# Performance work log

Hardware: AMD Instinct MI355X
Metric: run time of the kernel (lower is better)

Reference implementation:

```python
import jax, jax.numpy as jnp
import numpy as np
from jax import lax

# Module config (matches init_kwargs)
C_IN, C_OUT, D_STATE = 512, 256, 16
D_INNER = 2 * C_OUT          # canonical Mamba expand=2
DT_RANK = C_OUT // 16        # ceil(256/16) = 16
D_CONV = 4
BN_EPS = 1e-5


def setup_inputs() -> dict:
    key = jax.random.key(0)
    ks = jax.random.split(key, 16)
    s = 0.02
    B, H, W = 8, 64, 64
    inp = {
        "x": jax.random.normal(ks[0], (B, C_IN, H, W), jnp.float32),
        # lateral 1x1 conv
        "lateral_w": jax.random.normal(ks[1], (C_OUT, C_IN), jnp.float32) * s,
        "lateral_b": jnp.zeros((C_OUT,), jnp.float32),
        # mamba block params
        "in_proj_w": jax.random.normal(ks[2], (2 * D_INNER, C_OUT), jnp.float32) * s,
        "conv1d_w": jax.random.normal(ks[3], (D_INNER, D_CONV), jnp.float32) * s,
        "conv1d_b": jnp.zeros((D_INNER,), jnp.float32),
        "x_proj_w": jax.random.normal(ks[4], (DT_RANK + 2 * D_STATE, D_INNER), jnp.float32) * s,
        "dt_proj_w": jax.random.normal(ks[5], (D_INNER, DT_RANK), jnp.float32) * s,
        "dt_proj_b": jnp.full((D_INNER,), -4.0, jnp.float32),  # softplus -> small dt
        "A_log": jnp.log(jnp.broadcast_to(jnp.arange(1, D_STATE + 1, dtype=jnp.float32), (D_INNER, D_STATE))),  # S4D-real init
        "D_param": jnp.ones((D_INNER,), jnp.float32),
        "out_proj_w": jax.random.normal(ks[6], (C_OUT, D_INNER), jnp.float32) * s,
        # refine: 3x3 conv + BN (eval) + ReLU
        "refine_w": jax.random.normal(ks[7], (C_OUT, C_OUT, 3, 3), jnp.float32) * s,
        "refine_b": jnp.zeros((C_OUT,), jnp.float32),
        "bn_gamma": jnp.ones((C_OUT,), jnp.float32),
        "bn_beta": jnp.zeros((C_OUT,), jnp.float32),
        "bn_mean": jnp.zeros((C_OUT,), jnp.float32),
        "bn_var": jnp.ones((C_OUT,), jnp.float32),
    }
    return inp


def _silu(v):
    return v * jax.nn.sigmoid(v)


def _mamba(u, in_proj_w, conv1d_w, conv1d_b, x_proj_w, dt_proj_w, dt_proj_b,
           A_log, D_param, out_proj_w):
    """Canonical Mamba block on u: (B, L, D) -> (B, L, D)."""
    B, L, D = u.shape
    xz = jnp.einsum('bld,ed->ble', u, in_proj_w)            # (B,L,2*d_inner)
    xm, z = jnp.split(xz, 2, axis=-1)
    # causal depthwise conv1d over L
    xc = xm.transpose(0, 2, 1)                               # (B,d_inner,L)
    xc = lax.conv_general_dilated(xc, conv1d_w[:, None, :], (1,),
                                  [(D_CONV - 1, 0)],
                                  feature_group_count=D_INNER)
    xc = _silu(xc + conv1d_b[None, :, None]).transpose(0, 2, 1)  # (B,L,d_inner)
    proj = jnp.einsum('bld,ed->ble', xc, x_proj_w)           # (B,L,dt_rank+2*N)
    dt_r = proj[..., :DT_RANK]
    B_ssm = proj[..., DT_RANK:DT_RANK + D_STATE]             # (B,L,N)
    C_ssm = proj[..., DT_RANK + D_STATE:]                    # (B,L,N)
    dt = jax.nn.softplus(jnp.einsum('blr,dr->bld', dt_r, dt_proj_w) + dt_proj_b)
    A = -jnp.exp(A_log)                                      # (d_inner,N)

    def step(h, inputs):
        dt_t, B_t, C_t, x_t = inputs                         # (B,d), (B,N), (B,N), (B,d)
        dA = jnp.exp(dt_t[..., None] * A)                    # (B,d,N)
        h = dA * h + dt_t[..., None] * B_t[:, None, :] * x_t[..., None]
        y = jnp.einsum('bdn,bn->bd', h, C_t)
        return h, y

    xs = (dt.transpose(1, 0, 2), B_ssm.transpose(1, 0, 2),
          C_ssm.transpose(1, 0, 2), xc.transpose(1, 0, 2))
    h0 = jnp.zeros((B, D_INNER, D_STATE), u.dtype)
    _, ys = lax.scan(step, h0, xs)                           # (L,B,d_inner)
    y = ys.transpose(1, 0, 2) + xc * D_param
    y = y * _silu(z)
    return jnp.einsum('ble,de->bld', y, out_proj_w)          # (B,L,D)


def reference(x, lateral_w, lateral_b, in_proj_w, conv1d_w, conv1d_b, x_proj_w,
              dt_proj_w, dt_proj_b, A_log, D_param, out_proj_w, refine_w,
              refine_b, bn_gamma, bn_beta, bn_mean, bn_var):
    B, _, H, W = x.shape
    # lateral 1x1 conv
    xl = jnp.einsum('oi,bihw->bohw', lateral_w, x) + lateral_b[None, :, None, None]
    # mamba on flattened spatial sequence, residual add
    u = xl.reshape(B, C_OUT, H * W).transpose(0, 2, 1)        # (B,L,C)
    m = _mamba(u, in_proj_w, conv1d_w, conv1d_b, x_proj_w, dt_proj_w,
               dt_proj_b, A_log, D_param, out_proj_w)
    xr = xl + m.transpose(0, 2, 1).reshape(B, C_OUT, H, W)
    # refine: 3x3 conv + BN(eval) + ReLU
    r = lax.conv_general_dilated(xr, refine_w, (1, 1), [(1, 1), (1, 1)])
    r = r + refine_b[None, :, None, None]
    inv = bn_gamma / jnp.sqrt(bn_var + BN_EPS)
    r = (r - bn_mean[None, :, None, None]) * inv[None, :, None, None] + bn_beta[None, :, None, None]
    return jax.nn.relu(r)
```

## Files before the change

### kernel.cpp

```cpp
#include <hip/hip_runtime.h>
#include <math.h>

#define NB   8
#define CIN  512
#define COUT 256
#define DIN  512
#define LHW  4096
#define NCHK 64
#define CHL  64
#define PW   66
#define PPOS (PW*PW)

typedef __attribute__((ext_vector_type(8))) short bf16x8;
typedef __attribute__((ext_vector_type(4))) float f32x4;

__device__ __forceinline__ float siluf(float v)  { return v / (1.f + __expf(-v)); }
__device__ __forceinline__ float splusf(float v) { return v > 20.f ? v : log1pf(__expf(v)); }

__device__ __forceinline__ unsigned short f2b(float f) {
  union { float f; unsigned u; } v; v.f = f;
  unsigned r = v.u + 0x7fff + ((v.u >> 16) & 1);
  return (unsigned short)(r >> 16);
}
__device__ __forceinline__ float b2f(unsigned int u) {
  union { unsigned u; float f; } v; v.u = (u & 0xffffu) << 16; return v.f;
}

__device__ __forceinline__ void gload16(const unsigned short* g, unsigned short* l) {
  __builtin_amdgcn_global_load_lds(
      (const __attribute__((address_space(1))) unsigned int*)g,
      (__attribute__((address_space(3))) unsigned int*)l, 16, 0, 0);
}

#define WO1 131072
#define WO2 393216
#define WO3 425984
#define WO4 557056
__global__ __launch_bounds__(256)
void k_wprep(const float* __restrict__ lw, const float* __restrict__ ipw,
             const float* __restrict__ xpw, const float* __restrict__ opw,
             const float* __restrict__ rw, unsigned short* __restrict__ wb) {
  const int i = blockIdx.x * 256 + threadIdx.x;
  if (i < WO1)      wb[i] = f2b(lw[i]);
  else if (i < WO2) wb[i] = f2b(ipw[i - WO1]);
  else if (i < WO3) {
    const int j = i - WO2, row = j >> 9, col = j & 511;
    wb[i] = (row < 48) ? f2b(xpw[row * 512 + col]) : (unsigned short)0;
  }
  else if (i < WO4) wb[i] = f2b(opw[i - WO3]);
  else {
    const int j = i - WO4, o = j / 2304, kk = j % 2304;
    const int tap = kk >> 8, ch = kk & 255;
    wb[i] = f2b(rw[(o * 256 + ch) * 9 + tap]);
  }
}

__global__ __launch_bounds__(256)
void k_xpose(const float* __restrict__ x, unsigned short* __restrict__ xt) {
  __shared__ unsigned short Ts[64][80];
  const int b  = blockIdx.z;
  const int k0 = blockIdx.y * 64;
  const int l0 = blockIdx.x * 64;
  const int t  = threadIdx.x;
  const int tx = t & 15, ty = t >> 4;
#pragma unroll
  for (int r = 0; r < 4; ++r) {
    const int k = ty + r * 16;
    float4 v = *(const float4*)(x + ((size_t)b * CIN + k0 + k) * LHW + l0 + tx * 4);
    Ts[tx*4+0][k] = f2b(v.x);
    Ts[tx*4+1][k] = f2b(v.y);
    Ts[tx*4+2][k] = f2b(v.z);
    Ts[tx*4+3][k] = f2b(v.w);
  }
  __syncthreads();
  const int lr = t >> 2, kc = (t & 3) * 16;
  unsigned short* dst = xt + ((size_t)b * LHW + l0 + lr) * CIN + k0 + kc;
  *(uint4*)dst       = *(const uint4*)&Ts[lr][kc];
  *(uint4*)(dst + 8) = *(const uint4*)&Ts[lr][kc + 8];
}

template<int RSA, int RSB, int KTOT>
__device__ __forceinline__ void gemm_loop_128(
    const unsigned short* __restrict__ Ab, const unsigned short* __restrict__ Bb,
    unsigned short* As, unsigned short* Bs, int t, f32x4 acc[4][4]) {
  const int w = t >> 6, lane = t & 63;
  const int wm = w >> 1, wn = w & 1;
  const int arow = t >> 2, acol = (t & 3) * 8;
  const int fr = lane & 15, g8 = (lane >> 4) * 8;
  for (int k0 = 0; k0 < KTOT; k0 += 32) {
    __syncthreads();
    gload16(Ab + (size_t)arow * RSA + k0 + acol,        &As[w * 512]);
    gload16(Ab + (size_t)(64 + arow) * RSA + k0 + acol, &As[2048 + w * 512]);
    gload16(Bb + (size_t)arow * RSB + k0 + acol,        &Bs[w * 512]);
    gload16(Bb + (size_t)(64 + arow) * RSB + k0 + acol, &Bs[2048 + w * 512]);
    __syncthreads();
    bf16x8 af[4], bf[4];
#pragma unroll
    for (int f = 0; f < 4; ++f) {
      af[f] = *(const bf16x8*)&As[(wm*64 + f*16 + fr) * 32 + g8];
      bf[f] = *(const bf16x8*)&Bs[(wn*64 + f*16 + fr) * 32 + g8];
    }
#pragma unroll
    for (int i = 0; i < 4; ++i)
#pragma unroll
      for (int j = 0; j < 4; ++j)
        acc[i][j] = __builtin_amdgcn_mfma_f32_16x16x32_bf16(af[i], bf[j], acc[i][j], 0, 0, 0);
  }
}

__global__ __launch_bounds__(256)
void k_lat_mfma(const unsigned short* __restrict__ xt, const unsigned short* __restrict__ lwb,
                const float* __restrict__ lb, unsigned short* __restrict__ ub) {
  __shared__ __align__(16) unsigned short As[4096], Bs[4096];
  const int t = threadIdx.x, lane = t & 63, w = t >> 6;
  const int wm = w >> 1, wn = w & 1;
  const int b = blockIdx.z, m0 = blockIdx.y * 128, n0 = blockIdx.x * 128;
  f32x4 acc[4][4] = {};
  gemm_loop_128<512, 512, 512>(xt + ((size_t)b * LHW + m0) * 512,
                               lwb + (size_t)n0 * 512, As, Bs, t, acc);
  const int fr = lane & 15, q4 = (lane >> 4) * 4;
#pragma unroll
  for (int i = 0; i < 4; ++i) {
    const int l = m0 + wm*64 + i*16 + q4;
#pragma unroll
    for (int j = 0; j < 4; ++j) {
      const int o = n0 + wn*64 + j*16 + fr;
      const float bias = lb[o];
      unsigned short* dst = ub + ((size_t)b * LHW + l) * COUT + o;
#pragma unroll
      for (int q = 0; q < 4; ++q)
        dst[(size_t)q * COUT] = f2b(acc[i][j][q] + bias);
    }
  }
}

__global__ __launch_bounds__(256)
void k_inproj_mfma(const unsigned short* __restrict__ ub, const unsigned short* __restrict__ ipwb,
                   unsigned short* __restrict__ xm_b, unsigned short* __restrict__ zsb) {
  __shared__ __align__(16) unsigned short As[4096], Bs[4096];
  const int t = threadIdx.x, lane = t & 63, w = t >> 6;
  const int wm = w >> 1, wn = w & 1;
  const int b = blockIdx.z, m0 = blockIdx.y * 128, n0 = blockIdx.x * 128;
  f32x4 acc[4][4] = {};
  gemm_loop_128<256, 256, 256>(ub + ((size_t)b * LHW + m0) * 256,
                               ipwb + (size_t)n0 * 256, As, Bs, t, acc);
  const int fr = lane & 15, q4 = (lane >> 4) * 4;
  const bool isz = (n0 >= 512);
#pragma unroll
  for (int i = 0; i < 4; ++i) {
    const int l = m0 + wm*64 + i*16 + q4;
#pragma unroll
    for (int j = 0; j < 4; ++j) {
      const int e = n0 + wn*64 + j*16 + fr;
      if (isz) {
        unsigned short* dst = zsb + ((size_t)b * LHW + l) * DIN + (e - 512);
#pragma unroll
        for (int q = 0; q < 4; ++q)
          dst[(size_t)q * DIN] = f2b(siluf(acc[i][j][q]));
      } else {
        unsigned short* dst = xm_b + ((size_t)b * LHW + l) * DIN + e;
#pragma unroll
        for (int q = 0; q < 4; ++q)
          dst[(size_t)q * DIN] = f2b(acc[i][j][q]);
      }
    }
  }
}

__global__ __launch_bounds__(256)
void k_conv1d(const unsigned short* __restrict__ xm_b, const float* __restrict__ cw,
              const float* __restrict__ cb, unsigned short* __restrict__ xc_b) {
  const int tid = blockIdx.x * 256 + threadIdx.x;
  const int e8 = tid & 63;
  const int l  = (tid >> 6) & 4095;
  const int b  = tid >> 18;
  const int e0 = e8 * 8;
  float acc[8];
  *(float4*)&acc[0] = *(const float4*)(cb + e0);
  *(float4*)&acc[4] = *(const float4*)(cb + e0 + 4);
  float wv[8][4];
#pragma unroll
  for (int q = 0; q < 8; ++q) {
    float4 w4 = *(const float4*)(cw + (e0 + q) * 4);
    wv[q][0] = w4.x; wv[q][1] = w4.y; wv[q][2] = w4.z; wv[q][3] = w4.w;
  }
  const unsigned short* base = xm_b + (size_t)b * LHW * DIN + e0;
#pragma unroll
  for (int k = 0; k < 4; ++k) {
    const int ll = l - 3 + k;
    if (ll >= 0) {
      uint4 raw = *(const uint4*)(base + (size_t)ll * DIN);
      acc[0] = fmaf(b2f(raw.x),       wv[0][k], acc[0]);
      acc[1] = fmaf(b2f(raw.x >> 16), wv[1][k], acc[1]);
      acc[2] = fmaf(b2f(raw.y),       wv[2][k], acc[2]);
      acc[3] = fmaf(b2f(raw.y >> 16), wv[3][k], acc[3]);
      acc[4] = fmaf(b2f(raw.z),       wv[4][k], acc[4]);
      acc[5] = fmaf(b2f(raw.z >> 16), wv[5][k], acc[5]);
      acc[6] = fmaf(b2f(raw.w),       wv[6][k], acc[6]);
      acc[7] = fmaf(b2f(raw.w >> 16), wv[7][k], acc[7]);
    }
  }
  uint4 o;
  o.x = (unsigned)f2b(siluf(acc[0])) | ((unsigned)f2b(siluf(acc[1])) << 16);
  o.y = (unsigned)f2b(siluf(acc[2])) | ((unsigned)f2b(siluf(acc[3])) << 16);
  o.z = (unsigned)f2b(siluf(acc[4])) | ((unsigned)f2b(siluf(acc[5])) << 16);
  o.w = (unsigned)f2b(siluf(acc[6])) | ((unsigned)f2b(siluf(acc[7])) << 16);
  *(uint4*)(xc_b + ((size_t)b * LHW + l) * DIN + e0) = o;
}

__global__ __launch_bounds__(256)
void k_xproj_mfma(const unsigned short* __restrict__ xc_b, const unsigned short* __restrict__ xpwb,
                  float* __restrict__ proj) {
  __shared__ __align__(16) unsigned short As[4096], Bs[2048];
  const int t = threadIdx.x, lane = t & 63, w = t >> 6;
  const int wm = w >> 1, wn = w & 1;
  const int b = blockIdx.y, m0 = blockIdx.x * 128;
  const int arow = t >> 2, acol = (t & 3) * 8;
  const int fr = lane & 15, g8 = (lane >> 4) * 8;
  const unsigned short* Ab = xc_b + ((size_t)b * LHW + m0) * 512;
  f32x4 acc[4][2] = {};
  for (int k0 = 0; k0 < 512; k0 += 32) {
    __syncthreads();
    gload16(Ab + (size_t)arow * 512 + k0 + acol,        &As[w * 512]);
    gload16(Ab + (size_t)(64 + arow) * 512 + k0 + acol, &As[2048 + w * 512]);
    gload16(xpwb + (size_t)arow * 512 + k0 + acol,      &Bs[w * 512]);
    __syncthreads();
    bf16x8 af[4], bf[2];
#pragma unroll
    for (int f = 0; f < 4; ++f)
      af[f] = *(const bf16x8*)&As[(wm*64 + f*16 + fr) * 32 + g8];
#pragma unroll
    for (int f = 0; f < 2; ++f)
      bf[f] = *(const bf16x8*)&Bs[(wn*32 + f*16 + fr) * 32 + g8];
#pragma unroll
    for (int i = 0; i < 4; ++i)
#pragma unroll
      for (int j = 0; j < 2; ++j)
        acc[i][j] = __builtin_amdgcn_mfma_f32_16x16x32_bf16(af[i], bf[j], acc[i][j], 0, 0, 0);
  }
  const int q4 = (lane >> 4) * 4;
#pragma unroll
  for (int i = 0; i < 4; ++i) {
    const int l = m0 + wm*64 + i*16 + q4;
#pragma unroll
    for (int j = 0; j < 2; ++j) {
      const int col = wn*32 + j*16 + fr;
      if (col < 48) {
        float* dst = proj + ((size_t)b * LHW + l) * 48 + col;
#pragma unroll
        for (int q = 0; q < 4; ++q)
          dst[(size_t)q * 48] = acc[i][j][q];
      }
    }
  }
}

__global__ __launch_bounds__(512)
void k_dt(const float* __restrict__ proj, const float* __restrict__ dtpw,
          const float* __restrict__ dtpb, unsigned short* __restrict__ dtb) {
  __shared__ float prs[32 * 16];
  const int d = threadIdx.x;
  const size_t l0 = (size_t)blockIdx.x * 32;
  for (int i = d; i < 32 * 4; i += 512) {
    const int row = i >> 2, c4 = i & 3;
    *(float4*)&prs[row * 16 + c4 * 4] = *(const float4*)(proj + (l0 + row) * 48 + c4 * 4);
  }
  float w[16];
#pragma unroll
  for (int q = 0; q < 4; ++q)
    *(float4*)(&w[q*4]) = *(const float4*)(dtpw + d * 16 + q * 4);
  const float bias = dtpb[d];
  __syncthreads();
#pragma unroll 4
  for (int i = 0; i < 32; ++i) {
    const float* pr = &prs[i * 16];
    float4 r0 = *(const float4*)pr;
    float4 r1 = *(const float4*)(pr + 4);
    float4 r2 = *(const float4*)(pr + 8);
    float4 r3 = *(const float4*)(pr + 12);
    float a0 = fmaf(w[0], r0.x, fmaf(w[1],  r0.y, fmaf(w[2],  r0.z, w[3]  * r0.w)));
    float a1 = fmaf(w[4], r1.x, fmaf(w[5],  r1.y, fmaf(w[6],  r1.z, w[7]  * r1.w)));
    float a2 = fmaf(w[8], r2.x, fmaf(w[9],  r2.y, fmaf(w[10], r2.z, w[11] * r2.w)));
    float a3 = fmaf(w[12],r3.x, fmaf(w[13], r3.y, fmaf(w[14], r3.z, w[15] * r3.w)));
    dtb[(l0 + i) * 512 + d] = f2b(splusf(bias + ((a0 + a1) + (a2 + a3))));
  }
}

__global__ __launch_bounds__(512, 4)
void k_scanA(const float* __restrict__ proj, const unsigned short* __restrict__ dtb,
             const unsigned short* __restrict__ xc_b,
             const float* __restrict__ A_log, float* __restrict__ PS) {
  __shared__ float prs[CHL * 16];
  const int bx = blockIdx.x;
  const int b = bx >> 6, c = bx & 63;
  const int d = threadIdx.x;
  const size_t rbase = (size_t)b * LHW + c * CHL;
  for (int i = d; i < CHL * 4; i += 512) {
    const int row = i >> 2, c4 = i & 3;
    *(float4*)&prs[row * 16 + c4 * 4] = *(const float4*)(proj + (rbase + row) * 48 + 16 + c4 * 4);
  }
  float An[16], h[16];
#pragma unroll
  for (int q = 0; q < 4; ++q) {
    float4 a4 = *(const float4*)(A_log + d*16 + q*4);
    An[q*4+0] = -__expf(a4.x); An[q*4+1] = -__expf(a4.y);
    An[q*4+2] = -__expf(a4.z); An[q*4+3] = -__expf(a4.w);
  }
#pragma unroll
  for (int n = 0; n < 16; ++n) h[n] = 0.f;
  const float An0 = An[0];
  bool lin = true;
#pragma unroll
  for (int n = 1; n < 16; ++n)
    lin = lin && (fabsf(An[n] - (n + 1) * An0) <= 1e-4f * fabsf(An[n]));
  float sdt = 0.f;
  const unsigned short* dt0 = dtb + rbase * 512 + d;
  const unsigned short* xc0 = xc_b + rbase * DIN + d;
  __syncthreads();
  for (int i = 0; i < CHL; ++i) {
    const float dt = b2f(dt0[(size_t)i * 512]);
    sdt += dt;
    const float dtx = dt * b2f(xc0[(size_t)i * DIN]);
    float dA[16];
    if (lin) {
      const float e1 = __expf(dt * An0);
      const float e2 = e1 * e1, e3 = e2 * e1, e4 = e2 * e2;
      dA[0] = e1; dA[1] = e2; dA[2] = e3; dA[3] = e4;
#pragma unroll
      for (int n = 4; n < 16; ++n) dA[n] = dA[n-4] * e4;
    } else {
#pragma unroll
      for (int n = 0; n < 16; ++n) dA[n] = __expf(dt * An[n]);
    }
    const float* pr = &prs[i * 16];
#pragma unroll
    for (int q = 0; q < 4; ++q) {
      float4 B4 = *(const float4*)(pr + q*4);
      h[q*4+0] = fmaf(dA[q*4+0], h[q*4+0], dtx * B4.x);
      h[q*4+1] = fmaf(dA[q*4+1], h[q*4+1], dtx * B4.y);
      h[q*4+2] = fmaf(dA[q*4+2], h[q*4+2], dtx * B4.z);
      h[q*4+3] = fmaf(dA[q*4+3], h[q*4+3], dtx * B4.w);
    }
  }
  float* o = PS + ((size_t)bx * 512 + d) * 32;
#pragma unroll
  for (int q = 0; q < 4; ++q)
    *(float4*)(o + q*4) = make_float4(__expf(sdt*An[q*4+0]), __expf(sdt*An[q*4+1]),
                                      __expf(sdt*An[q*4+2]), __expf(sdt*An[q*4+3]));
#pragma unroll
  for (int q = 0; q < 4; ++q)
    *(float4*)(o + 16 + q*4) = make_float4(h[q*4], h[q*4+1], h[q*4+2], h[q*4+3]);
}

__global__ __launch_bounds__(256)
void k_scanB(const float* __restrict__ PS, float* __restrict__ hst) {
  const int tid = blockIdx.x * 256 + threadIdx.x;
  const int n = tid & 15;
  const int d = (tid >> 4) & 511;
  const int b = tid >> 13;
  float h = 0.f;
  for (int c = 0; c < NCHK; ++c) {
    const size_t idx = (size_t)((b*NCHK + c)*512 + d);
    hst[idx*16 + n] = h;
    h = PS[idx*32 + n] * h + PS[idx*32 + 16 + n];
  }
}

__global__ __launch_bounds__(512, 4)
void k_scanC(const float* __restrict__ proj, const unsigned short* __restrict__ dtb,
             const unsigned short* __restrict__ xc_b,
             const unsigned short* __restrict__ zsb, const float* __restrict__ hst,
             const float* __restrict__ A_log, const float* __restrict__ Dpar,
             unsigned short* __restrict__ ydata) {
  __shared__ float prs[CHL * 32];
  const int bx = blockIdx.x;
  const int b = bx >> 6, c = bx & 63;
  const int d = threadIdx.x;
  const size_t rbase = (size_t)b * LHW + c * CHL;
  for (int i = d; i < CHL * 8; i += 512) {
    const int row = i >> 3, c4 = i & 7;
    *(float4*)&prs[row * 32 + c4 * 4] = *(const float4*)(proj + (rbase + row) * 48 + 16 + c4 * 4);
  }
  float An[16], h[16];
#pragma unroll
  for (int q = 0; q < 4; ++q) {
    float4 a4 = *(const float4*)(A_log + d*16 + q*4);
    An[q*4+0] = -__expf(a4.x); An[q*4+1] = -__expf(a4.y);
    An[q*4+2] = -__expf(a4.z); An[q*4+3] = -__expf(a4.w);
  }
#pragma unroll
  for (int q = 0; q < 4; ++q) {
    float4 h4 = *(const float4*)(hst + ((size_t)bx * 512 + d) * 16 + q*4);
    h[q*4+0] = h4.x; h[q*4+1] = h4.y; h[q*4+2] = h4.z; h[q*4+3] = h4.w;
  }
  const float An0 = An[0];
  bool lin = true;
#pragma unroll
  for (int n = 1; n < 16; ++n)
    lin = lin && (fabsf(An[n] - (n + 1) * An0) <= 1e-4f * fabsf(An[n]));
  const float dp = Dpar[d];
  const unsigned short* dt0 = dtb + rbase * 512 + d;
  const unsigned short* xc0 = xc_b + rbase * DIN + d;
  const unsigned short* zs0 = zsb + rbase * DIN + d;
  unsigned short* y0 = ydata + rbase * DIN + d;
  __syncthreads();
  for (int i = 0; i < CHL; ++i) {
    const float dt = b2f(dt0[(size_t)i * 512]);
    const float xt = b2f(xc0[(size_t)i * DIN]);
    const float zv = b2f(zs0[(size_t)i * DIN]);
    const float dtx = dt * xt;
    float dA[16];
    if (lin) {
      const float e1 = __expf(dt * An0);
      const float e2 = e1 * e1, e3 = e2 * e1, e4 = e2 * e2;
      dA[0] = e1; dA[1] = e2; dA[2] = e3; dA[3] = e4;
#pragma unroll
      for (int n = 4; n < 16; ++n) dA[n] = dA[n-4] * e4;
    } else {
#pragma unroll
      for (int n = 0; n < 16; ++n) dA[n] = __expf(dt * An[n]);
    }
    const float* pr = &prs[i * 32];
    float y0a = 0.f, y1a = 0.f, y2a = 0.f, y3a = 0.f;
#pragma unroll
    for (int q = 0; q < 4; ++q) {
      float4 B4 = *(const float4*)(pr + q*4);
      float4 C4 = *(const float4*)(pr + 16 + q*4);
      h[q*4+0] = fmaf(dA[q*4+0], h[q*4+0], dtx * B4.x);
      h[q*4+1] = fmaf(dA[q*4+1], h[q*4+1], dtx * B4.y);
      h[q*4+2] = fmaf(dA[q*4+2], h[q*4+2], dtx * B4.z);
      h[q*4+3] = fmaf(dA[q*4+3], h[q*4+3], dtx * B4.w);
      y0a = fmaf(h[q*4+0], C4.x, y0a);
      y1a = fmaf(h[q*4+1], C4.y, y1a);
      y2a = fmaf(h[q*4+2], C4.z, y2a);
      y3a = fmaf(h[q*4+3], C4.w, y3a);
    }
    const float y = (y0a + y1a) + (y2a + y3a);
    y0[(size_t)i * DIN] = f2b((y + xt * dp) * zv);
  }
}

__global__ __launch_bounds__(256)
void k_outproj_mfma(const unsigned short* __restrict__ ydata, const unsigned short* __restrict__ opwb,
                    const unsigned short* __restrict__ ub, unsigned short* __restrict__ xrp) {
  __shared__ __align__(16) unsigned short As[4096], Bs[4096];
  const int t = threadIdx.x, lane = t & 63, w = t >> 6;
  const int wm = w >> 1, wn = w & 1;
  const int b = blockIdx.z, m0 = blockIdx.y * 128, n0 = blockIdx.x * 128;
  f32x4 acc[4][4] = {};
  gemm_loop_128<512, 512, 512>(ydata + ((size_t)b * LHW + m0) * 512,
                               opwb + (size_t)n0 * 512, As, Bs, t, acc);
  const int fr = lane & 15, q4 = (lane >> 4) * 4;
#pragma unroll
  for (int i = 0; i < 4; ++i) {
    const int lbase = m0 + wm*64 + i*16 + q4;
#pragma unroll
    for (int q = 0; q < 4; ++q) {
      const int l = lbase + q;
      const int pos = ((l >> 6) + 1) * PW + (l & 63) + 1;
#pragma unroll
      for (int j = 0; j < 4; ++j) {
        const int o = n0 + wn*64 + j*16 + fr;
        const float r = b2f(ub[((size_t)b * LHW + l) * COUT + o]);
        xrp[((size_t)b * PPOS + pos) * COUT + o] = f2b(acc[i][j][q] + r);
      }
    }
  }
}

__global__ __launch_bounds__(256)
void k_refine_mfma(const unsigned short* __restrict__ Aw,
                   const unsigned short* __restrict__ xrp,
                   const float* __restrict__ rb, const float* __restrict__ bng,
                   const float* __restrict__ bnb, const float* __restrict__ bnm,
                   const float* __restrict__ bnv, float* __restrict__ out) {
  __shared__ __align__(16) unsigned short As[4096], Bs[4096];
  const int t = threadIdx.x;
  const int lane = t & 63;
  const int w = t >> 6;
  const int wm = w >> 1, wn = w & 1;
  const int b  = blockIdx.z;
  const int m0 = blockIdx.y * 128;
  const int n0 = blockIdx.x * 128;
  const int y0 = n0 >> 6;
  const unsigned short* xb = xrp + (size_t)b * PPOS * COUT;
  const int arow = t >> 2;
  const int acol = (t & 3) * 8;
  f32x4 acc[4][4] = {};
  for (int ks = 0; ks < 72; ++ks) {
    const int tap = ks >> 3;
    const int i0  = (ks & 7) * 32;
    const int ky  = tap / 3, kx = tap - ky * 3;
    const int k0  = tap * 256 + i0;
    const unsigned short* ga0 = Aw + (size_t)(m0 + arow) * 2304 + k0 + acol;
    const unsigned short* gb0 = xb + ((size_t)((y0 + ky) * PW + kx + arow)) * COUT + i0 + acol;
    __syncthreads();
    gload16(ga0,              &As[w * 512]);
    gload16(ga0 + 64 * 2304,  &As[2048 + w * 512]);
    gload16(gb0,              &Bs[w * 512]);
    gload16(gb0 + PW * COUT,  &Bs[2048 + w * 512]);
    __syncthreads();
    const int fr = lane & 15, g8 = (lane >> 4) * 8;
    bf16x8 af[4], bfr[4];
#pragma unroll
    for (int f = 0; f < 4; ++f) {
      af[f]  = *(const bf16x8*)&As[(wm*64 + f*16 + fr) * 32 + g8];
      bfr[f] = *(const bf16x8*)&Bs[(wn*64 + f*16 + fr) * 32 + g8];
    }
#pragma unroll
    for (int i = 0; i < 4; ++i)
#pragma unroll
      for (int j = 0; j < 4; ++j)
        acc[i][j] = __builtin_amdgcn_mfma_f32_16x16x32_bf16(af[i], bfr[j], acc[i][j], 0, 0, 0);
  }
  const int fr = lane & 15, q4 = (lane >> 4) * 4;
#pragma unroll
  for (int i = 0; i < 4; ++i) {
    const int obase = m0 + wm*64 + i*16 + q4;
#pragma unroll
    for (int q = 0; q < 4; ++q) {
      const int o = obase + q;
      const float inv = bng[o] * rsqrtf(bnv[o] + 1e-5f);
      const float sh  = (rb[o] - bnm[o]) * inv + bnb[o];
      float* orow = out + ((size_t)b * COUT + o) * LHW + n0 + wn*64 + fr;
#pragma unroll
      for (int j = 0; j < 4; ++j)
        orow[j*16] = fmaxf(fmaf(acc[i][j][q], inv, sh), 0.f);
    }
  }
}

extern "C" void kernel_launch(void* const* d_in, const int* in_sizes, int n_in,
                              void* d_out, int out_size, void* d_ws, size_t ws_size,
                              hipStream_t stream) {
  const float* x    = (const float*)d_in[0];
  const float* lw   = (const float*)d_in[1];
  const float* lb   = (const float*)d_in[2];
  const float* ipw  = (const float*)d_in[3];
  const float* cw   = (const float*)d_in[4];
  const float* cb   = (const float*)d_in[5];
  const float* xpw  = (const float*)d_in[6];
  const float* dtpw = (const float*)d_in[7];
  const float* dtpb = (const float*)d_in[8];
  const float* Alog = (const float*)d_in[9];
  const float* Dpar = (const float*)d_in[10];
  const float* opw  = (const float*)d_in[11];
  const float* rw   = (const float*)d_in[12];
  const float* rb   = (const float*)d_in[13];
  const float* bng  = (const float*)d_in[14];
  const float* bnb  = (const float*)d_in[15];
  const float* bnm  = (const float*)d_in[16];
  const float* bnv  = (const float*)d_in[17];
  float* out = (float*)d_out;

  float* ws = (float*)d_ws;
  unsigned short* ub   = (unsigned short*)ws;
  unsigned short* xt   = (unsigned short*)(ws + 4194304);
  unsigned short* xm_b = (unsigned short*)(ws + 12582912);
  unsigned short* xc_b = (unsigned short*)(ws + 20971520);
  unsigned short* zsb  = (unsigned short*)(ws + 29360128);
  float* proj = ws + 46137344;
  float* PS   = ws + 47710208;
  float* hst  = ws + 56098816;
  unsigned short* wb = (unsigned short*)(ws + 60293120);
  unsigned short* lwb  = wb;
  unsigned short* ipwb = wb + WO1;
  unsigned short* xpwb = wb + WO2;
  unsigned short* opwb = wb + WO3;
  unsigned short* Aw   = wb + WO4;
  unsigned short* ydata = xm_b;
  unsigned short* dtb   = xt;
  unsigned short* xrp   = xt;

  k_wprep<<<dim3(4480), 256, 0, stream>>>(lw, ipw, xpw, opw, rw, wb);
  k_xpose<<<dim3(64, 8, 8), 256, 0, stream>>>(x, xt);
  k_lat_mfma<<<dim3(2, 32, 8), 256, 0, stream>>>(xt, lwb, lb, ub);
  k_inproj_mfma<<<dim3(8, 32, 8), 256, 0, stream>>>(ub, ipwb, xm_b, zsb);
  k_conv1d<<<dim3(8192), 256, 0, stream>>>(xm_b, cw, cb, xc_b);
  k_xproj_mfma<<<dim3(32, 8), 256, 0, stream>>>(xc_b, xpwb, proj);
  k_dt<<<dim3(NB * LHW / 32), 512, 0, stream>>>(proj, dtpw, dtpb, dtb);
  k_scanA<<<dim3(NB * NCHK), 512, 0, stream>>>(proj, dtb, xc_b, Alog, PS);
  k_scanB<<<dim3(256), 256, 0, stream>>>(PS, hst);
  k_scanC<<<dim3(NB * NCHK), 512, 0, stream>>>(proj, dtb, xc_b, zsb, hst, Alog, Dpar, ydata);
  hipMemsetAsync(xrp, 0, (size_t)NB * PPOS * COUT * sizeof(unsigned short), stream);
  k_outproj_mfma<<<dim3(2, 32, 8), 256, 0, stream>>>(ydata, opwb, ub, xrp);
  k_refine_mfma<<<dim3(32, 2, 8), 256, 0, stream>>>(Aw, xrp, rb, bng, bnb, bnm, bnv, out);
}
```

Before: 411.8 us.

## Fold dt_proj into x_proj weights, fuse dt GEMM, halve scan chunk length

A new prep kernel precomputes dt_proj_w·x_proj_w[:16] as a fused 512x512 bf16 weight, stacked on the B/C rows of x_proj. One MFMA GEMM then produces both softplus(dt) in bf16 and the B/C projections, which removes the separate k_dt kernel and its reread of proj. The cost is a larger GEMM (N padded to 640 instead of 64), and rounding the fused weights to bf16 changes dt numerics. Softplus is also rewritten in a stable max+log(1+exp(-|v|)) form, and the scan now uses 128 chunks of 32 to give more parallel blocks at the price of a longer serial carry pass.

```diff
diff --git a/kernel.cpp b/kernel.cpp
--- a/kernel.cpp
+++ b/kernel.cpp
@@ -6,8 +6,8 @@
 #define COUT 256
 #define DIN  512
 #define LHW  4096
-#define NCHK 64
-#define CHL  64
+#define NCHK 128
+#define CHL  32
 #define PW   66
 #define PPOS (PW*PW)
 
@@ -15,7 +15,9 @@
 typedef __attribute__((ext_vector_type(4))) float f32x4;
 
 __device__ __forceinline__ float siluf(float v)  { return v / (1.f + __expf(-v)); }
-__device__ __forceinline__ float splusf(float v) { return v > 20.f ? v : log1pf(__expf(v)); }
+__device__ __forceinline__ float splusf(float v) {
+  return fmaxf(v, 0.f) + __logf(1.f + __expf(-fabsf(v)));
+}
 
 __device__ __forceinline__ unsigned short f2b(float f) {
   union { float f; unsigned u; } v; v.f = f;
@@ -53,6 +55,22 @@
     const int tap = kk >> 8, ch = kk & 255;
     wb[i] = f2b(rw[(o * 256 + ch) * 9 + tap]);
   }
+}
+
+__global__ __launch_bounds__(256)
+void k_wfuse(const float* __restrict__ dtpw, const float* __restrict__ xpw,
+             unsigned short* __restrict__ wfb) {
+  const int tid = blockIdx.x * 256 + threadIdx.x;
+  const int row = tid >> 9, e = tid & 511;
+  float v = 0.f;
+  if (row < 512) {
+#pragma unroll
+    for (int r = 0; r < 16; ++r)
+      v = fmaf(dtpw[row * 16 + r], xpw[r * 512 + e], v);
+  } else if (row < 560) {
+    v = xpw[(row - 512) * 512 + e];
+  }
+  wfb[tid] = f2b(v);
 }
 
 __global__ __launch_bounds__(256)
@@ -209,80 +227,36 @@
 }
 
 __global__ __launch_bounds__(256)
-void k_xproj_mfma(const unsigned short* __restrict__ xc_b, const unsigned short* __restrict__ xpwb,
-                  float* __restrict__ proj) {
-  __shared__ __align__(16) unsigned short As[4096], Bs[2048];
+void k_xdt_mfma(const unsigned short* __restrict__ xc_b, const unsigned short* __restrict__ wfb,
+                const float* __restrict__ dtpb,
+                unsigned short* __restrict__ dtb, float* __restrict__ proj) {
+  __shared__ __align__(16) unsigned short As[4096], Bs[4096];
   const int t = threadIdx.x, lane = t & 63, w = t >> 6;
   const int wm = w >> 1, wn = w & 1;
-  const int b = blockIdx.y, m0 = blockIdx.x * 128;
-  const int arow = t >> 2, acol = (t & 3) * 8;
-  const int fr = lane & 15, g8 = (lane >> 4) * 8;
-  const unsigned short* Ab = xc_b + ((size_t)b * LHW + m0) * 512;
-  f32x4 acc[4][2] = {};
-  for (int k0 = 0; k0 < 512; k0 += 32) {
-    __syncthreads();
-    gload16(Ab + (size_t)arow * 512 + k0 + acol,        &As[w * 512]);
-    gload16(Ab + (size_t)(64 + arow) * 512 + k0 + acol, &As[2048 + w * 512]);
-    gload16(xpwb + (size_t)arow * 512 + k0 + acol,      &Bs[w * 512]);
-    __syncthreads();
-    bf16x8 af[4], bf[2];
-#pragma unroll
-    for (int f = 0; f < 4; ++f)
-      af[f] = *(const bf16x8*)&As[(wm*64 + f*16 + fr) * 32 + g8];
-#pragma unroll
-    for (int f = 0; f < 2; ++f)
-      bf[f] = *(const bf16x8*)&Bs[(wn*32 + f*16 + fr) * 32 + g8];
-#pragma unroll
-    for (int i = 0; i < 4; ++i)
-#pragma unroll
-      for (int j = 0; j < 2; ++j)
-        acc[i][j] = __builtin_amdgcn_mfma_f32_16x16x32_bf16(af[i], bf[j], acc[i][j], 0, 0, 0);
-  }
-  const int q4 = (lane >> 4) * 4;
+  const int b = blockIdx.z, m0 = blockIdx.x * 128, n0 = blockIdx.y * 128;
+  f32x4 acc[4][4] = {};
+  gemm_loop_128<512, 512, 512>(xc_b + ((size_t)b * LHW + m0) * 512,
+                               wfb + (size_t)n0 * 512, As, Bs, t, acc);
+  const int fr = lane & 15, q4 = (lane >> 4) * 4;
 #pragma unroll
   for (int i = 0; i < 4; ++i) {
     const int l = m0 + wm*64 + i*16 + q4;
 #pragma unroll
-    for (int j = 0; j < 2; ++j) {
-      const int col = wn*32 + j*16 + fr;
-      if (col < 48) {
-        float* dst = proj + ((size_t)b * LHW + l) * 48 + col;
+    for (int j = 0; j < 4; ++j) {
+      const int c = n0 + wn*64 + j*16 + fr;
+      if (c < 512) {
+        const float bias = dtpb[c];
+        unsigned short* dst = dtb + ((size_t)b * LHW + l) * 512 + c;
+#pragma unroll
+        for (int q = 0; q < 4; ++q)
+          dst[(size_t)q * 512] = f2b(splusf(acc[i][j][q] + bias));
+      } else if (c < 560) {
+        float* dst = proj + ((size_t)b * LHW + l) * 48 + (c - 512);
 #pragma unroll
         for (int q = 0; q < 4; ++q)
           dst[(size_t)q * 48] = acc[i][j][q];
       }
     }
-  }
-}
-
-__global__ __launch_bounds__(512)
-void k_dt(const float* __restrict__ proj, const float* __restrict__ dtpw,
-          const float* __restrict__ dtpb, unsigned short* __restrict__ dtb) {
-  __shared__ float prs[32 * 16];
-  const int d = threadIdx.x;
-  const size_t l0 = (size_t)blockIdx.x * 32;
-  for (int i = d; i < 32 * 4; i += 512) {
-    const int row = i >> 2, c4 = i & 3;
-    *(float4*)&prs[row * 16 + c4 * 4] = *(const float4*)(proj + (l0 + row) * 48 + c4 * 4);
-  }
-  float w[16];
-#pragma unroll
-  for (int q = 0; q < 4; ++q)
-    *(float4*)(&w[q*4]) = *(const float4*)(dtpw + d * 16 + q * 4);
-  const float bias = dtpb[d];
-  __syncthreads();
-#pragma unroll 4
-  for (int i = 0; i < 32; ++i) {
-    const float* pr = &prs[i * 16];
-    float4 r0 = *(const float4*)pr;
-    float4 r1 = *(const float4*)(pr + 4);
-    float4 r2 = *(const float4*)(pr + 8);
-    float4 r3 = *(const float4*)(pr + 12);
-    float a0 = fmaf(w[0], r0.x, fmaf(w[1],  r0.y, fmaf(w[2],  r0.z, w[3]  * r0.w)));
-    float a1 = fmaf(w[4], r1.x, fmaf(w[5],  r1.y, fmaf(w[6],  r1.z, w[7]  * r1.w)));
-    float a2 = fmaf(w[8], r2.x, fmaf(w[9],  r2.y, fmaf(w[10], r2.z, w[11] * r2.w)));
-    float a3 = fmaf(w[12],r3.x, fmaf(w[13], r3.y, fmaf(w[14], r3.z, w[15] * r3.w)));
-    dtb[(l0 + i) * 512 + d] = f2b(splusf(bias + ((a0 + a1) + (a2 + a3))));
   }
 }
 
@@ -292,7 +266,7 @@
              const float* __restrict__ A_log, float* __restrict__ PS) {
   __shared__ float prs[CHL * 16];
   const int bx = blockIdx.x;
-  const int b = bx >> 6, c = bx & 63;
+  const int b = bx >> 7, c = bx & 127;
   const int d = threadIdx.x;
   const size_t rbase = (size_t)b * LHW + c * CHL;
   for (int i = d; i < CHL * 4; i += 512) {
@@ -374,7 +348,7 @@
              unsigned short* __restrict__ ydata) {
   __shared__ float prs[CHL * 32];
   const int bx = blockIdx.x;
-  const int b = bx >> 6, c = bx & 63;
+  const int b = bx >> 7, c = bx & 127;
   const int d = threadIdx.x;
   const size_t rbase = (size_t)b * LHW + c * CHL;
   for (int i = d; i < CHL * 8; i += 512) {
@@ -559,13 +533,13 @@
   unsigned short* xm_b = (unsigned short*)(ws + 12582912);
   unsigned short* xc_b = (unsigned short*)(ws + 20971520);
   unsigned short* zsb  = (unsigned short*)(ws + 29360128);
-  float* proj = ws + 46137344;
-  float* PS   = ws + 47710208;
+  float* proj = ws + 37748736;
+  float* PS   = ws + 39321600;
   float* hst  = ws + 56098816;
-  unsigned short* wb = (unsigned short*)(ws + 60293120);
+  unsigned short* wb  = (unsigned short*)(ws + 64487424);
+  unsigned short* wfb = (unsigned short*)(ws + 65060864);
   unsigned short* lwb  = wb;
   unsigned short* ipwb = wb + WO1;
-  unsigned short* xpwb = wb + WO2;
   unsigned short* opwb = wb + WO3;
   unsigned short* Aw   = wb + WO4;
   unsigned short* ydata = xm_b;
@@ -573,12 +547,12 @@
   unsigned short* xrp   = xt;
 
   k_wprep<<<dim3(4480), 256, 0, stream>>>(lw, ipw, xpw, opw, rw, wb);
+  k_wfuse<<<dim3(1280), 256, 0, stream>>>(dtpw, xpw, wfb);
   k_xpose<<<dim3(64, 8, 8), 256, 0, stream>>>(x, xt);
   k_lat_mfma<<<dim3(2, 32, 8), 256, 0, stream>>>(xt, lwb, lb, ub);
   k_inproj_mfma<<<dim3(8, 32, 8), 256, 0, stream>>>(ub, ipwb, xm_b, zsb);
   k_conv1d<<<dim3(8192), 256, 0, stream>>>(xm_b, cw, cb, xc_b);
-  k_xproj_mfma<<<dim3(32, 8), 256, 0, stream>>>(xc_b, xpwb, proj);
-  k_dt<<<dim3(NB * LHW / 32), 512, 0, stream>>>(proj, dtpw, dtpb, dtb);
+  k_xdt_mfma<<<dim3(32, 5, 8), 256, 0, stream>>>(xc_b, wfb, dtpb, dtb, proj);
   k_scanA<<<dim3(NB * NCHK), 512, 0, stream>>>(proj, dtb, xc_b, Alog, PS);
   k_scanB<<<dim3(256), 256, 0, stream>>>(PS, hst);
   k_scanC<<<dim3(NB * NCHK), 512, 0, stream>>>(proj, dtb, xc_b, zsb, hst, Alog, Dpar, ydata);
```

Result: no change. 409.7 us (-0.5%).
